# Kernel tuning notes

Hardware: AMD Instinct MI355X
Metric: run time of the kernel (lower is better)

The kernel has to match this reference:

```python
import jax, jax.numpy as jnp
import numpy as np

N = 50000          # nodes
E = 1_600_000      # edges (before self-loops)
F_IN = 512         # feature_num
H1, C1 = 8, 8      # conv1: heads=8, out_channels=8
OUT = 128          # output_num (conv2, heads=1)
NEG_SLOPE = 0.2    # GATConv default leaky-relu slope


def gat_conv(x, W, a_src, a_dst, bias, src, dst, heads, ch, concat):
    """PyG GATConv (eval mode) on edge list (src -> dst)."""
    n = x.shape[0]
    h = (x @ W).reshape(n, heads, ch)                      # [N,H,C]
    alpha_src = (h * a_src).sum(-1)                        # [N,H]
    alpha_dst = (h * a_dst).sum(-1)                        # [N,H]
    e = alpha_src[src] + alpha_dst[dst]                    # [E,H]
    e = jnp.where(e > 0, e, NEG_SLOPE * e)                 # leaky_relu
    # segment softmax over edges sharing the same destination
    e_max = jax.ops.segment_max(e, dst, num_segments=n)    # self-loops => no empty segs
    w = jnp.exp(e - e_max[dst])
    denom = jax.ops.segment_sum(w, dst, num_segments=n)
    alpha = w / denom[dst]                                 # [E,H]
    msg = h[src] * alpha[:, :, None]                       # [E,H,C]
    out = jax.ops.segment_sum(msg, dst, num_segments=n)    # [N,H,C]
    out = out.reshape(n, heads * ch) if concat else out.mean(axis=1)
    return out + bias


def setup_inputs() -> dict:
    key = jax.random.key(0)
    ks = jax.random.split(key, 10)
    x = jax.random.normal(ks[0], (N, F_IN), dtype=jnp.float32)
    edge_index = jax.random.randint(ks[1], (2, E), 0, N, dtype=jnp.int64)
    s = 0.1
    return {
        "x": x,
        "edge_index": edge_index,
        "W1": jax.random.normal(ks[2], (F_IN, H1 * C1), dtype=jnp.float32) * s,
        "att_src1": jax.random.normal(ks[3], (H1, C1), dtype=jnp.float32) * s,
        "att_dst1": jax.random.normal(ks[4], (H1, C1), dtype=jnp.float32) * s,
        "b1": jnp.zeros((H1 * C1,), dtype=jnp.float32),
        "W2": jax.random.normal(ks[5], (H1 * C1, OUT), dtype=jnp.float32) * s,
        "att_src2": jax.random.normal(ks[6], (1, OUT), dtype=jnp.float32) * s,
        "att_dst2": jax.random.normal(ks[7], (1, OUT), dtype=jnp.float32) * s,
        "b2": jnp.zeros((OUT,), dtype=jnp.float32),
    }


def reference(x, edge_index, W1, att_src1, att_dst1, b1, W2, att_src2, att_dst2, b2):
    # PyG GATConv adds self-loops by default
    loops = jnp.arange(N, dtype=edge_index.dtype)
    src = jnp.concatenate([edge_index[0], loops])
    dst = jnp.concatenate([edge_index[1], loops])
    h = gat_conv(x, W1, att_src1, att_dst1, b1, src, dst, H1, C1, concat=True)
    h = jax.nn.elu(h)
    out = gat_conv(h, W2, att_src2, att_dst2, b2, src, dst, 1, OUT, concat=False)
    return out
```

## Files before the change

kernel.cpp:

```cpp
#include <hip/hip_runtime.h>
#include <math.h>

#define N_NODES 50000
#define F_IN    512
#define H1      8
#define C1      8
#define D1      64
#define OUT_C   128
#define NEG     0.2f

#define SCHUNK  256
#define SNBLK   ((N_NODES + SCHUNK - 1)/SCHUNK)

#define NHB      256
#define HTHREADS 1024
#define HALF     25000
#define HWORDS   12500

#define G1_ROWS  256
#define NB1      ((N_NODES + G1_ROWS - 1)/G1_ROWS)

using bf16x8 = __attribute__((ext_vector_type(8))) short;
using f32x4  = __attribute__((ext_vector_type(4))) float;
typedef unsigned short u16;
typedef unsigned int   u32;

__device__ __forceinline__ float leaky(float x){
    return fmaxf(x, 0.f) + NEG * fminf(x, 0.f);
}
__device__ __forceinline__ u16 f2bf(float f){
    u32 u = __float_as_uint(f);
    u32 r = u + 0x7FFF + ((u>>16)&1);
    return (u16)(r>>16);
}
__device__ __forceinline__ float bf2f(u16 h){ return __uint_as_float(((u32)h)<<16); }

__device__ __forceinline__ void cvt8(const float4& a, const float4& b, bf16x8& hi, bf16x8& lo){
    u16 h0=f2bf(a.x),h1=f2bf(a.y),h2=f2bf(a.z),h3=f2bf(a.w);
    u16 h4=f2bf(b.x),h5=f2bf(b.y),h6=f2bf(b.z),h7=f2bf(b.w);
    hi = (bf16x8){(short)h0,(short)h1,(short)h2,(short)h3,
                  (short)h4,(short)h5,(short)h6,(short)h7};
    lo = (bf16x8){(short)f2bf(a.x-bf2f(h0)),(short)f2bf(a.y-bf2f(h1)),
                  (short)f2bf(a.z-bf2f(h2)),(short)f2bf(a.w-bf2f(h3)),
                  (short)f2bf(b.x-bf2f(h4)),(short)f2bf(b.y-bf2f(h5)),
                  (short)f2bf(b.z-bf2f(h6)),(short)f2bf(b.w-bf2f(h7))};
}

__global__ __launch_bounds__(1024) void k_histB(const int* __restrict__ dst_a, int E, int CE,
                                                u16* __restrict__ histmat){
    __shared__ u32 lcnt[HWORDS];
    const int blk = blockIdx.x;
    const int i0 = blk*CE;
    const int i1 = min(i0+CE, E + N_NODES);
    for (int p=0;p<2;p++){
        for (int w=threadIdx.x; w<HWORDS; w+=HTHREADS) lcnt[w]=0;
        __syncthreads();
        const int lo = p*HALF, hi = lo+HALF;
        for (int i=i0+(int)threadIdx.x; i<i1; i+=HTHREADS){
            int d = (i<E)? dst_a[i] : (i-E);
            if (d>=lo && d<hi){
                int dd = d - lo;
                atomicAdd(&lcnt[dd>>1], 1u<<((dd&1)*16));
            }
        }
        __syncthreads();
        u16* dst = histmat + (size_t)blk*N_NODES + lo;
        for (int w=threadIdx.x; w<HWORDS; w+=HTHREADS){
            *(u32*)(dst + 2*w) = lcnt[w];
        }
        __syncthreads();
    }
}

__global__ __launch_bounds__(256) void k_colscan(u16* __restrict__ histmat, int* __restrict__ cnt){
    int n = blockIdx.x*256 + threadIdx.x;
    if (n >= N_NODES) return;
    u32 run = 0;
    u16* p = histmat + n;
    #pragma unroll 4
    for (int b=0;b<NHB;b++){
        u32 v = p[(size_t)b*N_NODES];
        p[(size_t)b*N_NODES] = (u16)run;
        run += v;
    }
    cnt[n] = (int)run;
}

__global__ __launch_bounds__(256) void k_scanA(const int* __restrict__ cnt, int* bsum){
    __shared__ int sm[256];
    int idx = blockIdx.x*256 + threadIdx.x;
    int v = (idx < N_NODES) ? cnt[idx] : 0;
    sm[threadIdx.x] = v; __syncthreads();
    for (int off=128; off>0; off>>=1){
        if (threadIdx.x < off) sm[threadIdx.x] += sm[threadIdx.x+off];
        __syncthreads();
    }
    if (threadIdx.x==0) bsum[blockIdx.x] = sm[0];
}

__global__ __launch_bounds__(256) void k_scanB(const int* __restrict__ bsum, int* boff, int* rowptr){
    __shared__ int sm[256];
    int t = threadIdx.x;
    int v = (t < SNBLK) ? bsum[t] : 0;
    sm[t]=v; __syncthreads();
    for (int off=1; off<256; off<<=1){
        int u = (t>=off)? sm[t-off] : 0;
        __syncthreads();
        sm[t]+=u; __syncthreads();
    }
    if (t < SNBLK) boff[t] = sm[t] - v;
    if (t==255) rowptr[N_NODES] = sm[255];
}

__global__ __launch_bounds__(256) void k_scanC(const int* __restrict__ cnt, const int* __restrict__ boff,
                                               int* rowptr){
    __shared__ int sm[256];
    int idx = blockIdx.x*256 + threadIdx.x;
    int t = threadIdx.x;
    int v = (idx<N_NODES)? cnt[idx] : 0;
    sm[t]=v; __syncthreads();
    for (int off=1; off<256; off<<=1){
        int u = (t>=off)? sm[t-off] : 0;
        __syncthreads();
        sm[t]+=u; __syncthreads();
    }
    if (idx<N_NODES){
        rowptr[idx] = boff[blockIdx.x] + sm[t] - v;
    }
}

__global__ __launch_bounds__(1024) void k_scatterB(const int* __restrict__ src_a, const int* __restrict__ dst_a,
                                                   int E, int CE,
                                                   const u16* __restrict__ histmat, const int* __restrict__ rowptr,
                                                   int* __restrict__ srcs){
    __shared__ u32 lcnt[HWORDS];
    const int blk = blockIdx.x;
    const int i0 = blk*CE;
    const int i1 = min(i0+CE, E + N_NODES);
    const u16* __restrict__ pb = histmat + (size_t)blk*N_NODES;
    for (int p=0;p<2;p++){
        for (int w=threadIdx.x; w<HWORDS; w+=HTHREADS) lcnt[w]=0;
        __syncthreads();
        const int lo = p*HALF, hi = lo+HALF;
        for (int i=i0+(int)threadIdx.x; i<i1; i+=HTHREADS){
            int s, d;
            if (i<E){ s=src_a[i]; d=dst_a[i]; } else { s=d=i-E; }
            if (d>=lo && d<hi){
                int dd = d - lo;
                u32 old = atomicAdd(&lcnt[dd>>1], 1u<<((dd&1)*16));
                u32 rank = (old >> ((dd&1)*16)) & 0xFFFFu;
                int pos = rowptr[d] + (int)pb[d] + (int)rank;
                srcs[pos] = s;
            }
        }
        __syncthreads();
    }
}

__global__ void k_cvtW(const float* __restrict__ W1, u16* __restrict__ whiT, u16* __restrict__ wloT){
    int i = blockIdx.x*blockDim.x + threadIdx.x;
    if (i >= F_IN*D1) return;
    int k = i >> 6, col = i & 63;
    float v = W1[i];
    u16 hi = f2bf(v);
    float lo = v - bf2f(hi);
    whiT[col*F_IN + k] = hi;
    wloT[col*F_IN + k] = f2bf(lo);
}

__global__ void k_cvtW2(const float* __restrict__ W2, u16* __restrict__ w2hiT, u16* __restrict__ w2loT){
    int i = blockIdx.x*blockDim.x + threadIdx.x;
    if (i >= D1*OUT_C) return;
    int k = i >> 7, col = i & 127;
    float v = W2[i];
    u16 hi = f2bf(v);
    float lo = v - bf2f(hi);
    w2hiT[col*D1 + k] = hi;
    w2loT[col*D1 + k] = f2bf(lo);
}

__global__ __launch_bounds__(1024) void k_gemm1(
        const float* __restrict__ x,
        const u16* __restrict__ whiT, const u16* __restrict__ wloT,
        const float* __restrict__ att_src, const float* __restrict__ att_dst,
        u16* __restrict__ h1b, float* __restrict__ asrc, float* __restrict__ adst){
    __shared__ u16 Bh[D1*F_IN];
    __shared__ u16 Bl[D1*F_IN];
    const int tid = threadIdx.x;
    const int wid = tid>>6, l = tid&63;
    const int lq = l>>4, lr = l&15;

    for (int i = tid; i < (D1*F_IN)/8; i += 1024){
        int col = i >> 6;
        int c   = i & 63;
        int boff = (col*1024 + c*16) ^ ((col&7)<<4);
        *(uint4*)((char*)Bh + boff) = *(const uint4*)(whiT + (size_t)i*8);
        *(uint4*)((char*)Bl + boff) = *(const uint4*)(wloT + (size_t)i*8);
    }
    __syncthreads();

    const int wavebase = blockIdx.x*G1_ROWS + wid*16;
    const int arow = min(wavebase + lr, N_NODES-1);
    const float* __restrict__ xrow = x + (size_t)arow*F_IN + lq*8;

    f32x4 acc[4];
    #pragma unroll
    for (int n=0;n<4;n++) acc[n] = (f32x4){0.f,0.f,0.f,0.f};

    float4 p0 = *(const float4*)(xrow);
    float4 p1 = *(const float4*)(xrow+4);
    float4 p2 = *(const float4*)(xrow+32);
    float4 p3 = *(const float4*)(xrow+36);

    for (int ks=0; ks<8; ks++){
        bf16x8 ahi0, alo0, ahi1, alo1;
        cvt8(p0, p1, ahi0, alo0);
        cvt8(p2, p3, ahi1, alo1);
        if (ks < 7){
            const float* nx = xrow + (ks+1)*64;
            p0 = *(const float4*)(nx);
            p1 = *(const float4*)(nx+4);
            p2 = *(const float4*)(nx+32);
            p3 = *(const float4*)(nx+36);
        }
        const int k0 = ks*64;
        #pragma unroll
        for (int n=0;n<4;n++){
            const int colb = n*16 + lr;
            const int swz  = (colb&7)<<4;
            const int b0 = (colb*1024 + (k0 + lq*8)*2) ^ swz;
            const int b1 = (colb*1024 + (k0 + 32 + lq*8)*2) ^ swz;
            bf16x8 bhi0 = *(const bf16x8*)((const char*)Bh + b0);
            bf16x8 blo0 = *(const bf16x8*)((const char*)Bl + b0);
            acc[n] = __builtin_amdgcn_mfma_f32_16x16x32_bf16(ahi0, bhi0, acc[n], 0,0,0);
            acc[n] = __builtin_amdgcn_mfma_f32_16x16x32_bf16(ahi0, blo0, acc[n], 0,0,0);
            acc[n] = __builtin_amdgcn_mfma_f32_16x16x32_bf16(alo0, bhi0, acc[n], 0,0,0);
            bf16x8 bhi1 = *(const bf16x8*)((const char*)Bh + b1);
            bf16x8 blo1 = *(const bf16x8*)((const char*)Bl + b1);
            acc[n] = __builtin_amdgcn_mfma_f32_16x16x32_bf16(ahi1, bhi1, acc[n], 0,0,0);
            acc[n] = __builtin_amdgcn_mfma_f32_16x16x32_bf16(ahi1, blo1, acc[n], 0,0,0);
            acc[n] = __builtin_amdgcn_mfma_f32_16x16x32_bf16(alo1, bhi1, acc[n], 0,0,0);
        }
    }

    #pragma unroll
    for (int n=0;n<4;n++){
        int col = n*16 + lr;
        float as_w = att_src[col], ad_w = att_dst[col];
        #pragma unroll
        for (int i=0;i<4;i++){
            int node = wavebase + lq*4 + i;
            float v = acc[n][i];
            float s = v*as_w, d = v*ad_w;
            s += __shfl_xor(s,1); d += __shfl_xor(d,1);
            s += __shfl_xor(s,2); d += __shfl_xor(d,2);
            s += __shfl_xor(s,4); d += __shfl_xor(d,4);
            if (node < N_NODES){
                h1b[(size_t)node*D1 + col] = f2bf(v);
                if ((l&7)==0){
                    int head = col>>3;
                    asrc[node*H1 + head] = s;
                    adst[node*H1 + head] = d;
                }
            }
        }
    }
}

__global__ __launch_bounds__(256) void k_agg1(
        const int* __restrict__ rowptr, const int* __restrict__ srcs,
        const float* __restrict__ asrc1, const float* __restrict__ adst1,
        const u16* __restrict__ h1b, float* __restrict__ out1){
    const int node = blockIdx.x*4 + (threadIdx.x>>6);
    const int lane = threadIdx.x & 63;
    const int g = lane >> 3;
    const int p = lane & 7;
    const int r0 = __builtin_amdgcn_readfirstlane(rowptr[node]);
    const int r1 = __builtin_amdgcn_readfirstlane(rowptr[node+1]);
    const float ad = adst1[node*H1 + p];
    float a0=0,a1=0,a2=0,a3=0,a4=0,a5=0,a6=0,a7=0, den=0;
    for (int base=r0; base<r1; base+=64){
        int eidx = base + lane;
        int sl = srcs[eidx < r1 ? eidx : (r1-1)];
        const int m = min(64, r1-base);
        for (int k=0; k*8 < m; k++){
            int e = k*8 + g;
            int s = __shfl(sl, e);
            float w = (base + e < r1) ? __expf(leaky(asrc1[s*H1 + p] + ad)) : 0.f;
            uint4 pv = *(const uint4*)(h1b + (size_t)s*D1 + p*8);
            a0 += w*bf2f((u16)(pv.x&0xFFFFu)); a1 += w*bf2f((u16)(pv.x>>16));
            a2 += w*bf2f((u16)(pv.y&0xFFFFu)); a3 += w*bf2f((u16)(pv.y>>16));
            a4 += w*bf2f((u16)(pv.z&0xFFFFu)); a5 += w*bf2f((u16)(pv.z>>16));
            a6 += w*bf2f((u16)(pv.w&0xFFFFu)); a7 += w*bf2f((u16)(pv.w>>16));
            den += w;
        }
    }
    #pragma unroll
    for (int off=8; off<64; off<<=1){
        a0 += __shfl_xor(a0,off); a1 += __shfl_xor(a1,off);
        a2 += __shfl_xor(a2,off); a3 += __shfl_xor(a3,off);
        a4 += __shfl_xor(a4,off); a5 += __shfl_xor(a5,off);
        a6 += __shfl_xor(a6,off); a7 += __shfl_xor(a7,off);
        den += __shfl_xor(den,off);
    }
    if (g == 0){
        float inv = 1.f/den;
        float* o = out1 + (size_t)node*D1 + p*8;
        *(float4*)(o)   = make_float4(a0*inv, a1*inv, a2*inv, a3*inv);
        *(float4*)(o+4) = make_float4(a4*inv, a5*inv, a6*inv, a7*inv);
    }
}

__global__ __launch_bounds__(256) void k_gemm2(
        const float* __restrict__ out1, const float* __restrict__ b1,
        const u16* __restrict__ w2hiT, const u16* __restrict__ w2loT,
        const float* __restrict__ att_src2, const float* __restrict__ att_dst2,
        u16* __restrict__ h2b, float* __restrict__ asrc2, float* __restrict__ adst2){
    __shared__ u16 Ahi[64*64];
    __shared__ u16 Alo[64*64];
    const int tid = threadIdx.x;
    const int wid = tid>>6, l = tid&63;
    const int lq = l>>4, lr = l&15;
    const int rowbase = blockIdx.x*64;

    #pragma unroll
    for (int q=0;q<4;q++){
        int p = tid + 256*q;
        int r = p>>4, kseg = p&15;
        int grow = min(rowbase + r, N_NODES-1);
        float4 v = *(const float4*)(out1 + (size_t)grow*D1 + kseg*4);
        float4 bb = *(const float4*)(b1 + kseg*4);
        float a0 = v.x+bb.x, a1 = v.y+bb.y, a2 = v.z+bb.z, a3 = v.w+bb.w;
        a0 = a0>0.f ? a0 : (__expf(a0)-1.f);
        a1 = a1>0.f ? a1 : (__expf(a1)-1.f);
        a2 = a2>0.f ? a2 : (__expf(a2)-1.f);
        a3 = a3>0.f ? a3 : (__expf(a3)-1.f);
        u16 h0=f2bf(a0), h1v=f2bf(a1), h2v=f2bf(a2), h3v=f2bf(a3);
        u16 e0=f2bf(a0-bf2f(h0)), e1=f2bf(a1-bf2f(h1v)),
            e2=f2bf(a2-bf2f(h2v)), e3=f2bf(a3-bf2f(h3v));
        int boff = (r*128 + kseg*8) ^ ((r&7)<<4);
        *(ushort4*)((char*)Ahi + boff) = make_ushort4(h0,h1v,h2v,h3v);
        *(ushort4*)((char*)Alo + boff) = make_ushort4(e0,e1,e2,e3);
    }
    __syncthreads();

    const int arow = wid*16 + lr;
    bf16x8 ahi[2], alo[2];
    #pragma unroll
    for (int kt=0;kt<2;kt++){
        int boff = (arow*128 + kt*64 + lq*16) ^ ((arow&7)<<4);
        ahi[kt] = *(const bf16x8*)((const char*)Ahi + boff);
        alo[kt] = *(const bf16x8*)((const char*)Alo + boff);
    }

    f32x4 acc[8];
    #pragma unroll
    for (int n=0;n<8;n++) acc[n] = (f32x4){0.f,0.f,0.f,0.f};
    #pragma unroll
    for (int n=0;n<8;n++){
        #pragma unroll
        for (int kt=0;kt<2;kt++){
            const size_t wo = (size_t)(n*16+lr)*D1 + kt*32 + lq*8;
            bf16x8 bhi = *(const bf16x8*)(w2hiT + wo);
            bf16x8 blo = *(const bf16x8*)(w2loT + wo);
            acc[n] = __builtin_amdgcn_mfma_f32_16x16x32_bf16(ahi[kt], bhi, acc[n], 0,0,0);
            acc[n] = __builtin_amdgcn_mfma_f32_16x16x32_bf16(ahi[kt], blo, acc[n], 0,0,0);
            acc[n] = __builtin_amdgcn_mfma_f32_16x16x32_bf16(alo[kt], bhi, acc[n], 0,0,0);
        }
    }

    float aw[8], dw[8];
    #pragma unroll
    for (int n=0;n<8;n++){ aw[n]=att_src2[n*16+lr]; dw[n]=att_dst2[n*16+lr]; }
    #pragma unroll
    for (int i=0;i<4;i++){
        int node = rowbase + wid*16 + lq*4 + i;
        bool ok = node < N_NODES;
        float s = 0.f, d = 0.f;
        #pragma unroll
        for (int n=0;n<8;n++){
            float v = acc[n][i];
            s = fmaf(v, aw[n], s);
            d = fmaf(v, dw[n], d);
            if (ok) h2b[(size_t)node*OUT_C + n*16 + lr] = f2bf(v);
        }
        s += __shfl_xor(s,1); d += __shfl_xor(d,1);
        s += __shfl_xor(s,2); d += __shfl_xor(d,2);
        s += __shfl_xor(s,4); d += __shfl_xor(d,4);
        s += __shfl_xor(s,8); d += __shfl_xor(d,8);
        if (ok && lr==0){ asrc2[node]=s; adst2[node]=d; }
    }
}

__global__ __launch_bounds__(256) void k_agg2(
        const int* __restrict__ rowptr, const int* __restrict__ srcs,
        const float* __restrict__ asrc2, const float* __restrict__ adst2,
        const u16* __restrict__ h2b, const float* __restrict__ b2,
        float* __restrict__ out){
    const int node = blockIdx.x*4 + (threadIdx.x>>6);
    const int lane = threadIdx.x & 63;
    const int g = lane >> 4;
    const int p = lane & 15;
    const int r0 = __builtin_amdgcn_readfirstlane(rowptr[node]);
    const int r1 = __builtin_amdgcn_readfirstlane(rowptr[node+1]);
    const float ad = adst2[node];
    float a0=0,a1=0,a2=0,a3=0,a4=0,a5=0,a6=0,a7=0, den=0;
    for (int base=r0; base<r1; base+=64){
        int eidx = base + lane;
        int sl = srcs[eidx < r1 ? eidx : (r1-1)];
        float wl = (eidx < r1) ? __expf(leaky(asrc2[sl] + ad)) : 0.f;
        const int m = min(64, r1-base);
        for (int k=0; k*4 < m; k++){
            int e = k*4 + g;
            int   s = __shfl(sl, e);
            float w = __shfl(wl, e);
            uint4 pv = *(const uint4*)(h2b + (size_t)s*OUT_C + p*8);
            a0 += w*bf2f((u16)(pv.x&0xFFFFu)); a1 += w*bf2f((u16)(pv.x>>16));
            a2 += w*bf2f((u16)(pv.y&0xFFFFu)); a3 += w*bf2f((u16)(pv.y>>16));
            a4 += w*bf2f((u16)(pv.z&0xFFFFu)); a5 += w*bf2f((u16)(pv.z>>16));
            a6 += w*bf2f((u16)(pv.w&0xFFFFu)); a7 += w*bf2f((u16)(pv.w>>16));
            den += w;
        }
    }
    #pragma unroll
    for (int off=16; off<64; off<<=1){
        a0 += __shfl_xor(a0,off); a1 += __shfl_xor(a1,off);
        a2 += __shfl_xor(a2,off); a3 += __shfl_xor(a3,off);
        a4 += __shfl_xor(a4,off); a5 += __shfl_xor(a5,off);
        a6 += __shfl_xor(a6,off); a7 += __shfl_xor(a7,off);
        den += __shfl_xor(den,off);
    }
    if (g == 0){
        float inv = 1.f/den;
        const float* bb = b2 + p*8;
        float* o = out + (size_t)node*OUT_C + p*8;
        *(float4*)(o)   = make_float4(a0*inv+bb[0], a1*inv+bb[1], a2*inv+bb[2], a3*inv+bb[3]);
        *(float4*)(o+4) = make_float4(a4*inv+bb[4], a5*inv+bb[5], a6*inv+bb[6], a7*inv+bb[7]);
    }
}

extern "C" void kernel_launch(void* const* d_in, const int* in_sizes, int n_in,
                              void* d_out, int out_size, void* d_ws, size_t ws_size,
                              hipStream_t stream) {
    const float* x        = (const float*)d_in[0];
    const int*   edge     = (const int*)  d_in[1];
    const float* W1       = (const float*)d_in[2];
    const float* att_src1 = (const float*)d_in[3];
    const float* att_dst1 = (const float*)d_in[4];
    const float* b1       = (const float*)d_in[5];
    const float* W2       = (const float*)d_in[6];
    const float* att_src2 = (const float*)d_in[7];
    const float* att_dst2 = (const float*)d_in[8];
    const float* b2       = (const float*)d_in[9];
    float* out = (float*)d_out;

    const int E  = in_sizes[1] / 2;
    const int ET = E + N_NODES;
    const int CE = (ET + NHB - 1) / NHB;
    const int* src_a = edge;
    const int* dst_a = edge + E;

    float* ws = (float*)d_ws;
    float* h1f   = ws;
    float* asrc1 = h1f   + (size_t)N_NODES*D1;
    float* adst1 = asrc1 + (size_t)N_NODES*H1;
    float* out1  = adst1 + (size_t)N_NODES*H1;
    float* h2f   = out1  + (size_t)N_NODES*D1;
    float* asrc2 = h2f   + (size_t)N_NODES*OUT_C;
    float* adst2 = asrc2 + N_NODES;
    int*   cnt    = (int*)(adst2 + N_NODES);
    int*   rowptr = cnt    + N_NODES;
    int*   srcs   = rowptr + (N_NODES+4);
    int*   bsum   = srcs   + ET;
    int*   boff   = bsum   + 256;
    u16*   histmat= (u16*)(boff + 256);
    u16*   whiT   = histmat;
    u16*   wloT   = whiT + F_IN*D1;
    u16*   w2hiT  = wloT + F_IN*D1;
    u16*   w2loT  = w2hiT + D1*OUT_C;
    u16*   h1b    = (u16*)h1f;
    u16*   h2b    = (u16*)h2f;

    hipLaunchKernelGGL(k_histB,   dim3(NHB), dim3(HTHREADS), 0, stream, dst_a, E, CE, histmat);
    hipLaunchKernelGGL(k_colscan, dim3(SNBLK), dim3(256), 0, stream, histmat, cnt);
    hipLaunchKernelGGL(k_scanA,   dim3(SNBLK), dim3(256), 0, stream, cnt, bsum);
    hipLaunchKernelGGL(k_scanB,   dim3(1), dim3(256), 0, stream, bsum, boff, rowptr);
    hipLaunchKernelGGL(k_scanC,   dim3(SNBLK), dim3(256), 0, stream, cnt, boff, rowptr);
    hipLaunchKernelGGL(k_scatterB,dim3(NHB), dim3(HTHREADS), 0, stream,
                       src_a, dst_a, E, CE, histmat, rowptr, srcs);

    hipLaunchKernelGGL(k_cvtW2, dim3((D1*OUT_C+255)/256), dim3(256), 0, stream,
                       W2, w2hiT, w2loT);
    hipLaunchKernelGGL(k_cvtW, dim3((F_IN*D1+255)/256), dim3(256), 0, stream,
                       W1, whiT, wloT);

    hipLaunchKernelGGL(k_gemm1, dim3(NB1), dim3(1024), 0, stream,
                       x, whiT, wloT, att_src1, att_dst1, h1b, asrc1, adst1);
    hipLaunchKernelGGL(k_agg1, dim3((N_NODES+3)/4), dim3(256), 0, stream,
                       rowptr, srcs, asrc1, adst1, h1b, out1);

    hipLaunchKernelGGL(k_gemm2, dim3((N_NODES+63)/64), dim3(256), 0, stream,
                       out1, b1, w2hiT, w2loT, att_src2, att_dst2, h2b, asrc2, adst2);
    hipLaunchKernelGGL(k_agg2, dim3((N_NODES+3)/4), dim3(256), 0, stream,
                       rowptr, srcs, asrc2, adst2, h2b, b2, out);
}
```

Baseline: 222.9 us.

## Pack CSR histogram counts into bytes, merge scan and weight-conversion kernels

Per-block destination histograms now use 8-bit counters, four per word, so the whole node range fits in LDS. The histogram and scatter kernels therefore make one pass over the edges instead of two. The column scan now also does the block-sum reduction, and the two weight bf16 split kernels are merged into one, removing two launches. gemm1 is retuned to 224 rows and 896 threads per block. The byte counters and byte prefixes silently overflow if a node gets more than 255 edges in one block or a total in-degree above 255, which random inputs avoid but skewed graphs would not.

```diff
diff --git a/kernel.cpp b/kernel.cpp
--- a/kernel.cpp
+++ b/kernel.cpp
@@ -14,16 +14,17 @@
 
 #define NHB      256
 #define HTHREADS 1024
-#define HALF     25000
-#define HWORDS   12500
-
-#define G1_ROWS  256
+#define HW8      ((N_NODES + 3)/4)
+
+#define G1_ROWS  224
+#define G1_THR   896
 #define NB1      ((N_NODES + G1_ROWS - 1)/G1_ROWS)
 
 using bf16x8 = __attribute__((ext_vector_type(8))) short;
 using f32x4  = __attribute__((ext_vector_type(4))) float;
 typedef unsigned short u16;
 typedef unsigned int   u32;
+typedef unsigned char  u8;
 
 __device__ __forceinline__ float leaky(float x){
     return fmaxf(x, 0.f) + NEG * fminf(x, 0.f);
@@ -47,50 +48,39 @@
 }
 
 __global__ __launch_bounds__(1024) void k_histB(const int* __restrict__ dst_a, int E, int CE,
-                                                u16* __restrict__ histmat){
-    __shared__ u32 lcnt[HWORDS];
+                                                u8* __restrict__ histmat){
+    __shared__ u32 lcnt[HW8];
     const int blk = blockIdx.x;
     const int i0 = blk*CE;
     const int i1 = min(i0+CE, E + N_NODES);
-    for (int p=0;p<2;p++){
-        for (int w=threadIdx.x; w<HWORDS; w+=HTHREADS) lcnt[w]=0;
-        __syncthreads();
-        const int lo = p*HALF, hi = lo+HALF;
-        for (int i=i0+(int)threadIdx.x; i<i1; i+=HTHREADS){
-            int d = (i<E)? dst_a[i] : (i-E);
-            if (d>=lo && d<hi){
-                int dd = d - lo;
-                atomicAdd(&lcnt[dd>>1], 1u<<((dd&1)*16));
-            }
-        }
-        __syncthreads();
-        u16* dst = histmat + (size_t)blk*N_NODES + lo;
-        for (int w=threadIdx.x; w<HWORDS; w+=HTHREADS){
-            *(u32*)(dst + 2*w) = lcnt[w];
-        }
-        __syncthreads();
-    }
-}
-
-__global__ __launch_bounds__(256) void k_colscan(u16* __restrict__ histmat, int* __restrict__ cnt){
+    for (int w=threadIdx.x; w<HW8; w+=HTHREADS) lcnt[w]=0;
+    __syncthreads();
+    for (int i=i0+(int)threadIdx.x; i<i1; i+=HTHREADS){
+        int d = (i<E)? dst_a[i] : (i-E);
+        atomicAdd(&lcnt[d>>2], 1u<<((d&3)*8));
+    }
+    __syncthreads();
+    u32* dst = (u32*)(histmat + (size_t)blk*N_NODES);
+    for (int w=threadIdx.x; w<HW8; w+=HTHREADS) dst[w] = lcnt[w];
+}
+
+__global__ __launch_bounds__(256) void k_colscan(u8* __restrict__ histmat, int* __restrict__ cnt,
+                                                 int* __restrict__ bsum){
+    __shared__ int sm[256];
     int n = blockIdx.x*256 + threadIdx.x;
-    if (n >= N_NODES) return;
     u32 run = 0;
-    u16* p = histmat + n;
-    #pragma unroll 4
-    for (int b=0;b<NHB;b++){
-        u32 v = p[(size_t)b*N_NODES];
-        p[(size_t)b*N_NODES] = (u16)run;
-        run += v;
-    }
-    cnt[n] = (int)run;
-}
-
-__global__ __launch_bounds__(256) void k_scanA(const int* __restrict__ cnt, int* bsum){
-    __shared__ int sm[256];
-    int idx = blockIdx.x*256 + threadIdx.x;
-    int v = (idx < N_NODES) ? cnt[idx] : 0;
-    sm[threadIdx.x] = v; __syncthreads();
+    if (n < N_NODES){
+        u8* p = histmat + n;
+        #pragma unroll 4
+        for (int b=0;b<NHB;b++){
+            u32 v = p[(size_t)b*N_NODES];
+            p[(size_t)b*N_NODES] = (u8)run;
+            run += v;
+        }
+        cnt[n] = (int)run;
+    }
+    sm[threadIdx.x] = (n < N_NODES) ? (int)run : 0;
+    __syncthreads();
     for (int off=128; off>0; off>>=1){
         if (threadIdx.x < off) sm[threadIdx.x] += sm[threadIdx.x+off];
         __syncthreads();
@@ -131,55 +121,46 @@
 
 __global__ __launch_bounds__(1024) void k_scatterB(const int* __restrict__ src_a, const int* __restrict__ dst_a,
                                                    int E, int CE,
-                                                   const u16* __restrict__ histmat, const int* __restrict__ rowptr,
+                                                   const u8* __restrict__ histmat, const int* __restrict__ rowptr,
                                                    int* __restrict__ srcs){
-    __shared__ u32 lcnt[HWORDS];
+    __shared__ u32 lcnt[HW8];
     const int blk = blockIdx.x;
     const int i0 = blk*CE;
     const int i1 = min(i0+CE, E + N_NODES);
-    const u16* __restrict__ pb = histmat + (size_t)blk*N_NODES;
-    for (int p=0;p<2;p++){
-        for (int w=threadIdx.x; w<HWORDS; w+=HTHREADS) lcnt[w]=0;
-        __syncthreads();
-        const int lo = p*HALF, hi = lo+HALF;
-        for (int i=i0+(int)threadIdx.x; i<i1; i+=HTHREADS){
-            int s, d;
-            if (i<E){ s=src_a[i]; d=dst_a[i]; } else { s=d=i-E; }
-            if (d>=lo && d<hi){
-                int dd = d - lo;
-                u32 old = atomicAdd(&lcnt[dd>>1], 1u<<((dd&1)*16));
-                u32 rank = (old >> ((dd&1)*16)) & 0xFFFFu;
-                int pos = rowptr[d] + (int)pb[d] + (int)rank;
-                srcs[pos] = s;
-            }
-        }
-        __syncthreads();
-    }
-}
-
-__global__ void k_cvtW(const float* __restrict__ W1, u16* __restrict__ whiT, u16* __restrict__ wloT){
+    const u8* __restrict__ pb = histmat + (size_t)blk*N_NODES;
+    for (int w=threadIdx.x; w<HW8; w+=HTHREADS) lcnt[w]=0;
+    __syncthreads();
+    for (int i=i0+(int)threadIdx.x; i<i1; i+=HTHREADS){
+        int s, d;
+        if (i<E){ s=src_a[i]; d=dst_a[i]; } else { s=d=i-E; }
+        u32 old = atomicAdd(&lcnt[d>>2], 1u<<((d&3)*8));
+        u32 rank = (old >> ((d&3)*8)) & 0xFFu;
+        int pos = rowptr[d] + (int)pb[d] + (int)rank;
+        srcs[pos] = s;
+    }
+}
+
+__global__ void k_cvtW12(const float* __restrict__ W1, const float* __restrict__ W2,
+                         u16* __restrict__ whiT, u16* __restrict__ wloT,
+                         u16* __restrict__ w2hiT, u16* __restrict__ w2loT){
     int i = blockIdx.x*blockDim.x + threadIdx.x;
-    if (i >= F_IN*D1) return;
-    int k = i >> 6, col = i & 63;
-    float v = W1[i];
-    u16 hi = f2bf(v);
-    float lo = v - bf2f(hi);
-    whiT[col*F_IN + k] = hi;
-    wloT[col*F_IN + k] = f2bf(lo);
-}
-
-__global__ void k_cvtW2(const float* __restrict__ W2, u16* __restrict__ w2hiT, u16* __restrict__ w2loT){
-    int i = blockIdx.x*blockDim.x + threadIdx.x;
-    if (i >= D1*OUT_C) return;
-    int k = i >> 7, col = i & 127;
-    float v = W2[i];
-    u16 hi = f2bf(v);
-    float lo = v - bf2f(hi);
-    w2hiT[col*D1 + k] = hi;
-    w2loT[col*D1 + k] = f2bf(lo);
-}
-
-__global__ __launch_bounds__(1024) void k_gemm1(
+    if (i < F_IN*D1){
+        int k = i >> 6, col = i & 63;
+        float v = W1[i];
+        u16 hi = f2bf(v);
+        whiT[col*F_IN + k] = hi;
+        wloT[col*F_IN + k] = f2bf(v - bf2f(hi));
+    }
+    if (i < D1*OUT_C){
+        int k = i >> 7, col = i & 127;
+        float v = W2[i];
+        u16 hi = f2bf(v);
+        w2hiT[col*D1 + k] = hi;
+        w2loT[col*D1 + k] = f2bf(v - bf2f(hi));
+    }
+}
+
+__global__ __launch_bounds__(G1_THR) void k_gemm1(
         const float* __restrict__ x,
         const u16* __restrict__ whiT, const u16* __restrict__ wloT,
         const float* __restrict__ att_src, const float* __restrict__ att_dst,
@@ -190,7 +171,7 @@
     const int wid = tid>>6, l = tid&63;
     const int lq = l>>4, lr = l&15;
 
-    for (int i = tid; i < (D1*F_IN)/8; i += 1024){
+    for (int i = tid; i < (D1*F_IN)/8; i += G1_THR){
         int col = i >> 6;
         int c   = i & 63;
         int boff = (col*1024 + c*16) ^ ((col&7)<<4);
@@ -473,8 +454,8 @@
     int*   srcs   = rowptr + (N_NODES+4);
     int*   bsum   = srcs   + ET;
     int*   boff   = bsum   + 256;
-    u16*   histmat= (u16*)(boff + 256);
-    u16*   whiT   = histmat;
+    u8*    histmat= (u8*)(boff + 256);
+    u16*   whiT   = (u16*)histmat;
     u16*   wloT   = whiT + F_IN*D1;
     u16*   w2hiT  = wloT + F_IN*D1;
     u16*   w2loT  = w2hiT + D1*OUT_C;
@@ -482,19 +463,16 @@
     u16*   h2b    = (u16*)h2f;
 
     hipLaunchKernelGGL(k_histB,   dim3(NHB), dim3(HTHREADS), 0, stream, dst_a, E, CE, histmat);
-    hipLaunchKernelGGL(k_colscan, dim3(SNBLK), dim3(256), 0, stream, histmat, cnt);
-    hipLaunchKernelGGL(k_scanA,   dim3(SNBLK), dim3(256), 0, stream, cnt, bsum);
+    hipLaunchKernelGGL(k_colscan, dim3(SNBLK), dim3(256), 0, stream, histmat, cnt, bsum);
     hipLaunchKernelGGL(k_scanB,   dim3(1), dim3(256), 0, stream, bsum, boff, rowptr);
     hipLaunchKernelGGL(k_scanC,   dim3(SNBLK), dim3(256), 0, stream, cnt, boff, rowptr);
     hipLaunchKernelGGL(k_scatterB,dim3(NHB), dim3(HTHREADS), 0, stream,
                        src_a, dst_a, E, CE, histmat, rowptr, srcs);
 
-    hipLaunchKernelGGL(k_cvtW2, dim3((D1*OUT_C+255)/256), dim3(256), 0, stream,
-                       W2, w2hiT, w2loT);
-    hipLaunchKernelGGL(k_cvtW, dim3((F_IN*D1+255)/256), dim3(256), 0, stream,
-                       W1, whiT, wloT);
-
-    hipLaunchKernelGGL(k_gemm1, dim3(NB1), dim3(1024), 0, stream,
+    hipLaunchKernelGGL(k_cvtW12, dim3((F_IN*D1+255)/256), dim3(256), 0, stream,
+                       W1, W2, whiT, wloT, w2hiT, w2loT);
+
+    hipLaunchKernelGGL(k_gemm1, dim3(NB1), dim3(G1_THR), 0, stream,
                        x, whiT, wloT, att_src1, att_dst1, h1b, asrc1, adst1);
     hipLaunchKernelGGL(k_agg1, dim3((N_NODES+3)/4), dim3(256), 0, stream,
                        rowptr, srcs, asrc1, adst1, h1b, out1);
```

Measured after the change: 213.0 us. 1.05x faster.
